# Optimization experiments

Hardware: AMD Instinct MI355X
Metric: run time of the kernel (lower is better)

The kernel has to match this reference:

```python
import jax, jax.numpy as jnp
import numpy as np

B, S, D = 4, 4096, 1024
H, DK, DV = 8, 128, 128
SEG = 512
DH = 4096
EPS = 1e-5


def setup_inputs() -> dict:
    key = jax.random.key(0)
    ks = jax.random.split(key, 8)
    n = lambda k, shp, sc: (jax.random.normal(k, shp, jnp.float32) * sc)
    return {
        "x": n(ks[0], (B, S, D), 1.0),
        "ln_gamma": jnp.ones((D,), jnp.float32),
        "ln_beta": jnp.zeros((D,), jnp.float32),
        "Wq": n(ks[1], (D, H * DK), 0.02),
        "Wk": n(ks[2], (D, H * DK), 0.02),
        "Wv": n(ks[3], (D, H * DV), 0.02),
        "Wo": n(ks[4], (H * DV, D), 0.02),
        "betas": n(ks[5], (1, H, 1, DV), 1.0),
        "ff_w1": n(ks[6], (D, DH), 0.02),
        "ff_b1": jnp.zeros((DH,), jnp.float32),
        "ff_w2": n(ks[7], (DH, D), 0.02),
        "ff_b2": jnp.zeros((D,), jnp.float32),
    }


def layer_norm(x, gamma, beta):
    mu = x.mean(-1, keepdims=True)
    var = x.var(-1, keepdims=True)
    return (x - mu) * jax.lax.rsqrt(var + EPS) * gamma + beta


def gelu_tanh(x):
    c = np.sqrt(2.0 / np.pi).astype(np.float32)
    return 0.5 * x * (1.0 + jnp.tanh(c * (x + 0.044715 * x * x * x)))


def infini_attention(x, Wq, Wk, Wv, Wo, betas):
    b, s, _ = x.shape
    nseg = s // SEG

    def proj(W, dh):
        # (b,s,H*dh) -> (nseg, b, H, SEG, dh)
        y = (x @ W).reshape(b, nseg, SEG, H, dh)
        return y.transpose(1, 0, 3, 2, 4)

    q = proj(Wq, DK)
    k = proj(Wk, DK)
    v = proj(Wv, DV)

    gate = jax.nn.sigmoid(betas)  # (1,H,1,DV)
    scale = 1.0 / np.sqrt(DK).astype(np.float32)
    causal_mask = jnp.tril(jnp.ones((SEG, SEG), bool))

    def step(carry, qkv):
        mem, z = carry  # (b,H,DK,DV), (b,H,DK,1)
        qs, ks_, vs = qkv  # (b,H,SEG,dk/dv)
        sq = jax.nn.elu(qs) + 1.0
        # compressive-memory retrieval
        att_mem = (sq @ mem) / (sq @ z)  # (b,H,SEG,DV)
        # local (segment) dot-product attention
        scores = jnp.einsum("bhqk,bhsk->bhqs", qs, ks_) * scale
        scores = jnp.where(causal_mask, scores, -jnp.inf)
        att = jax.nn.softmax(scores, axis=-1) @ vs  # (b,H,SEG,DV)
        # linear memory update
        sk = jax.nn.elu(ks_) + 1.0
        mem = mem + jnp.einsum("bhsk,bhsv->bhkv", sk, vs)
        z = z + sk.sum(axis=2)[..., None]
        out = gate * att_mem + (1.0 - gate) * att
        return (mem, z), out

    mem0 = jnp.zeros((b, H, DK, DV), x.dtype)
    z0 = jnp.ones((b, H, DK, 1), x.dtype) / DK
    _, outs = jax.lax.scan(step, (mem0, z0), (q, k, v))
    # (nseg,b,H,SEG,DV) -> (b,s,H*DV)
    outs = outs.transpose(1, 0, 3, 2, 4).reshape(b, s, H * DV)
    return outs @ Wo


def reference(x, ln_gamma, ln_beta, Wq, Wk, Wv, Wo, betas, ff_w1, ff_b1, ff_w2, ff_b2):
    h = layer_norm(x, ln_gamma, ln_beta)
    x = x + infini_attention(h, Wq, Wk, Wv, Wo, betas)
    h = layer_norm(x, ln_gamma, ln_beta)
    ff = gelu_tanh(h @ ff_w1 + ff_b1) @ ff_w2 + ff_b2
    return x + ff
```

## Files before the change

kernel.cpp:

```cpp
#include <hip/hip_runtime.h>

typedef unsigned short u16;
typedef unsigned int   u32;
typedef float f32x4 __attribute__((ext_vector_type(4)));
typedef short bf16x8 __attribute__((ext_vector_type(8)));

#define DEV static __device__ __forceinline__

DEV u16 f2b(float f){
  u32 u = __builtin_bit_cast(u32, f);
  return (u16)((u + 0x7fffu + ((u >> 16) & 1u)) >> 16);
}
DEV float b2f(u16 h){ u32 u = ((u32)h) << 16; return __builtin_bit_cast(float, u); }
DEV u32 pack2(float a, float b){ return (u32)f2b(a) | ((u32)f2b(b) << 16); }
DEV uint4 pack8(const float* f){
  uint4 r; r.x = pack2(f[0],f[1]); r.y = pack2(f[2],f[3]);
  r.z = pack2(f[4],f[5]); r.w = pack2(f[6],f[7]); return r;
}
DEV void unpack8(uint4 u, float* f){
  f[0]=b2f((u16)(u.x&0xffffu)); f[1]=b2f((u16)(u.x>>16));
  f[2]=b2f((u16)(u.y&0xffffu)); f[3]=b2f((u16)(u.y>>16));
  f[4]=b2f((u16)(u.z&0xffffu)); f[5]=b2f((u16)(u.z>>16));
  f[6]=b2f((u16)(u.w&0xffffu)); f[7]=b2f((u16)(u.w>>16));
}
DEV float gelu_t(float x){
  const float z2 = 1.5957691216057308f*(x + 0.044715f*x*x*x);
  return x / (1.f + __expf(-z2));
}
DEV void g2l16(const u16* g, u16* l){
  __builtin_amdgcn_global_load_lds(
    (const __attribute__((address_space(1))) u32*)g,
    (__attribute__((address_space(3))) u32*)l, 16, 0, 0);
}

__global__ __launch_bounds__(256)
void ln_k(const float* __restrict__ x, const float* __restrict__ gamma,
          const float* __restrict__ beta, u16* __restrict__ out)
{
  const int row = blockIdx.x;
  const int t = threadIdx.x;
  const float4 v = ((const float4*)(x + (size_t)row*1024))[t];
  float s  = v.x+v.y+v.z+v.w;
  float ss = v.x*v.x+v.y*v.y+v.z*v.z+v.w*v.w;
  #pragma unroll
  for (int o=32;o;o>>=1){ s += __shfl_xor(s,o); ss += __shfl_xor(ss,o); }
  __shared__ float rs[4], rq[4];
  if ((t&63)==0){ rs[t>>6]=s; rq[t>>6]=ss; }
  __syncthreads();
  s  = rs[0]+rs[1]+rs[2]+rs[3];
  ss = rq[0]+rq[1]+rq[2]+rq[3];
  const float mean = s*(1.f/1024.f);
  const float var  = ss*(1.f/1024.f) - mean*mean;
  const float inv  = rsqrtf(var + 1e-5f);
  const float4 g4 = ((const float4*)gamma)[t];
  const float4 b4 = ((const float4*)beta)[t];
  float o[4];
  o[0]=(v.x-mean)*inv*g4.x+b4.x; o[1]=(v.y-mean)*inv*g4.y+b4.y;
  o[2]=(v.z-mean)*inv*g4.z+b4.z; o[3]=(v.w-mean)*inv*g4.w+b4.w;
  uint2 w; w.x = pack2(o[0],o[1]); w.y = pack2(o[2],o[3]);
  *(uint2*)(out + (size_t)row*1024 + t*4) = w;
}

__global__ __launch_bounds__(256)
void wconv_k(const float* __restrict__ W, u16* __restrict__ WT, int K, int N)
{
  __shared__ float tile[32][33];
  const int k0 = blockIdx.y<<5, n0 = blockIdx.x<<5;
  const int tx = threadIdx.x & 31, ty = threadIdx.x >> 5;
  #pragma unroll
  for (int r=0;r<32;r+=8)
    tile[ty+r][tx] = W[(size_t)(k0+ty+r)*N + n0+tx];
  __syncthreads();
  #pragma unroll
  for (int r=0;r<32;r+=8)
    WT[(size_t)(n0+ty+r)*K + k0+tx] = f2b(tile[tx][ty+r]);
}

#define EPI_QKV  0
#define EPI_WO   1
#define EPI_GELU 2
#define EPI_FF2  3

template<int EPI>
__global__ __launch_bounds__(512)
void gemm3_k(const u16* __restrict__ A, const u16* __restrict__ BT,
             int K, int lda, int ldb, int N,
             u16* __restrict__ obf, float* __restrict__ of32,
             const float* __restrict__ res, const float* __restrict__ bias)
{
  __shared__ __align__(16) u16 SA[2*4096];
  __shared__ __align__(16) u16 SB[2*8192];
  const int t = threadIdx.x, wid = t>>6, lane = t&63;
  const int c = lane&15, g = lane>>4;
  const int wm = wid>>2, wn = wid&3;
  const int nwg = gridDim.x*gridDim.y;
  const int lb = blockIdx.y*gridDim.x + blockIdx.x;
  const int nl = (lb&7)*(nwg>>3) + (lb>>3);
  const int bx = nl % gridDim.x, by = nl / gridDim.x;
  const int m0 = by<<7, n0 = bx<<8;
  const int srow = lane>>2;
  const int scol = (lane&3)<<3;
  const int sxor = (srow&3)<<3;
  const int rowA = (wid<<4) + srow;
  const u16* aSrc  = A  + (size_t)(m0 + rowA)*lda + (scol ^ sxor);
  const u16* bSrc0 = BT + (size_t)(n0 + rowA)*ldb + (scol ^ sxor);
  const u16* bSrc1 = BT + (size_t)(n0 + 128 + rowA)*ldb + (scol ^ sxor);
  const int kx = (g<<3) ^ ((c&3)<<3);

  f32x4 acc[4][4];
  const f32x4 zz = {0.f,0.f,0.f,0.f};
  #pragma unroll
  for (int i=0;i<4;i++){ acc[i][0]=zz; acc[i][1]=zz; acc[i][2]=zz; acc[i][3]=zz; }

  g2l16(aSrc,  &SA[wid<<9]);
  g2l16(bSrc0, &SB[wid<<9]);
  g2l16(bSrc1, &SB[(wid<<9) + 4096]);
  __syncthreads();

  const int nt = K >> 5;
  for (int tt = 0; tt < nt; ++tt){
    const int cur = tt & 1;
    if (tt + 1 < nt){
      const int ko = (tt+1) << 5;
      g2l16(aSrc + ko,  &SA[((cur^1)<<12) + (wid<<9)]);
      g2l16(bSrc0 + ko, &SB[((cur^1)<<13) + (wid<<9)]);
      g2l16(bSrc1 + ko, &SB[((cur^1)<<13) + (wid<<9) + 4096]);
    }
    bf16x8 af[4], bf[4];
    #pragma unroll
    for (int i=0;i<4;i++)
      af[i] = *(const bf16x8*)&SA[(cur<<12) + ((wm<<6)+(i<<4)+c)*32 + kx];
    #pragma unroll
    for (int j=0;j<4;j++)
      bf[j] = *(const bf16x8*)&SB[(cur<<13) + ((wn<<6)+(j<<4)+c)*32 + kx];
    #pragma unroll
    for (int i=0;i<4;i++)
      #pragma unroll
      for (int j=0;j<4;j++)
        acc[i][j] = __builtin_amdgcn_mfma_f32_16x16x32_bf16(af[i], bf[j], acc[i][j], 0,0,0);
    __syncthreads();
  }

  #pragma unroll
  for (int i=0;i<4;i++){
    const int gr0 = m0 + (wm<<6) + (i<<4) + (g<<2);
    #pragma unroll
    for (int j=0;j<4;j++){
      const int gc = n0 + (wn<<6) + (j<<4) + c;
      #pragma unroll
      for (int r=0;r<4;r++){
        const int gr = gr0 + r;
        const float vv = acc[i][j][r];
        if (EPI==EPI_QKV){
          obf[((size_t)(gc>>10)<<24) + (size_t)gr*1024 + (gc&1023)] = f2b(vv);
        } else if (EPI==EPI_WO){
          const size_t idx = (size_t)gr*N + gc;
          of32[idx] = res[idx] + vv;
        } else if (EPI==EPI_GELU){
          obf[(size_t)gr*N + gc] = f2b(gelu_t(vv + bias[gc]));
        } else {
          const size_t idx = (size_t)gr*N + gc;
          of32[idx] = of32[idx] + vv + (bias ? bias[gc] : 0.f);
        }
      }
    }
  }
}

__global__ __launch_bounds__(256)
void memseg_k(const u16* __restrict__ kb, const u16* __restrict__ vb,
              float* __restrict__ Mseg, float* __restrict__ zseg)
{
  const int bid = blockIdx.x;
  const int seg = bid & 7, h = (bid>>3)&7, b = bid>>6;
  __shared__ __align__(16) u16 Kt[128*64];
  __shared__ __align__(16) u16 Vt[128*64];
  const int t=threadIdx.x, w=t>>6, lane=t&63, c=lane&15, g=lane>>4;

  f32x4 acc[2][8];
  f32x4 zacc[2];
  const f32x4 zzero = {0.f,0.f,0.f,0.f};
  #pragma unroll
  for (int d=0;d<2;d++){ zacc[d]=zzero;
    #pragma unroll
    for (int j=0;j<8;j++) acc[d][j]=zzero; }
  bf16x8 bones;
  { u16 tmp[8];
    #pragma unroll
    for (int e=0;e<8;e++) tmp[e] = (c==0) ? (u16)0x3F80 : (u16)0;
    bones = __builtin_bit_cast(bf16x8, *(uint4*)tmp); }

  for (int s0=0; s0<512; s0+=64){
    __syncthreads();
    {
      const int s = lane, dk0 = w<<5;
      const size_t grow = ((size_t)b*4096 + seg*512 + s0 + s)*1024 + h*128 + dk0;
      #pragma unroll
      for (int jj=0;jj<4;jj++){
        float kf[8], vf[8];
        unpack8(*(const uint4*)(kb + grow + jj*8), kf);
        unpack8(*(const uint4*)(vb + grow + jj*8), vf);
        #pragma unroll
        for (int e=0;e<8;e++){
          const int dk = dk0 + jj*8 + e;
          const float ek = kf[e]>0.f ? kf[e]+1.f : __expf(kf[e]);
          Kt[(dk<<6) + (s ^ ((dk&7)<<3))] = f2b(ek);
          Vt[(dk<<6) + (s ^ ((dk&7)<<3))] = f2b(vf[e]);
        }
      }
    }
    __syncthreads();
    #pragma unroll
    for (int ks=0;ks<2;ks++){
      const int kc = (ks<<5) + (g<<3);
      const bf16x8 a0 = *(const bf16x8*)&Kt[((((w<<1)  )*16 + c)<<6) + (kc ^ ((c&7)<<3))];
      const bf16x8 a1 = *(const bf16x8*)&Kt[((((w<<1)+1)*16 + c)<<6) + (kc ^ ((c&7)<<3))];
      zacc[0] = __builtin_amdgcn_mfma_f32_16x16x32_bf16(a0, bones, zacc[0], 0,0,0);
      zacc[1] = __builtin_amdgcn_mfma_f32_16x16x32_bf16(a1, bones, zacc[1], 0,0,0);
      #pragma unroll
      for (int j=0;j<8;j++){
        const bf16x8 bv = *(const bf16x8*)&Vt[(((j<<4) + c)<<6) + (kc ^ ((c&7)<<3))];
        acc[0][j] = __builtin_amdgcn_mfma_f32_16x16x32_bf16(a0, bv, acc[0][j], 0,0,0);
        acc[1][j] = __builtin_amdgcn_mfma_f32_16x16x32_bf16(a1, bv, acc[1][j], 0,0,0);
      }
    }
  }
  const size_t mb = (size_t)bid*16384;
  #pragma unroll
  for (int d=0;d<2;d++){
    const int dk = ((w<<1)+d)*16 + (g<<2);
    #pragma unroll
    for (int j=0;j<8;j++)
      #pragma unroll
      for (int r=0;r<4;r++)
        Mseg[mb + (size_t)(dk + r)*128 + (j<<4) + c] = acc[d][j][r];
    if (c==0){
      #pragma unroll
      for (int r=0;r<4;r++) zseg[(size_t)bid*128 + dk + r] = zacc[d][r];
    }
  }
}

__global__ __launch_bounds__(256)
void scan_k(const float* __restrict__ Mseg, const float* __restrict__ zseg,
            u16* __restrict__ memBT, float* __restrict__ zB)
{
  const int bh = blockIdx.x >> 3, oct = blockIdx.x & 7;
  const int t = threadIdx.x;
  const int dv = (oct<<4) + (t&15);
  const int kd0 = (t>>4)<<3;
  float run[8];
  #pragma unroll
  for (int i=0;i<8;i++) run[i]=0.f;
  for (int seg=0; seg<8; seg++){
    const size_t base = ((size_t)bh*8 + seg)*16384;
    u16 tmp[8];
    #pragma unroll
    for (int i=0;i<8;i++) tmp[i] = f2b(run[i]);
    *(uint4*)(memBT + base + (size_t)dv*128 + kd0) = *(const uint4*)tmp;
    #pragma unroll
    for (int i=0;i<8;i++) run[i] += Mseg[base + (size_t)(kd0+i)*128 + dv];
  }
  if (oct==0 && t < 128){
    float zr = 1.f/128.f;
    for (int seg=0; seg<8; seg++){
      const size_t base = ((size_t)bh*8 + seg)*128;
      zB[base + t] = zr;
      zr += zseg[base + t];
    }
  }
}

__global__ __launch_bounds__(256,2)
void attn_k(const u16* __restrict__ qb, const u16* __restrict__ kb,
            const u16* __restrict__ vb, const u16* __restrict__ memBT,
            const float* __restrict__ zB, const float* __restrict__ betas,
            u16* __restrict__ attc)
{
  const int bid = blockIdx.x;
  const int s = bid & 255, rt = 7 - (bid >> 8);
  const int seg = s&7, h=(s>>3)&7, b=s>>6;
  __shared__ __align__(16) u16 smem[16384];
  __shared__ __align__(16) u16 Ps[4096];
  u16* Ks = smem;
  u16* Vt = smem + 8192;
  float* zP = (float*)Ps;
  const int t=threadIdx.x, w=t>>6, lane=t&63, c=lane&15, g=lane>>4;
  const size_t base = ((size_t)b*4096 + seg*512)*1024 + h*128;

  bf16x8 af[4];
  {
    const u16* qsrc = qb + base + (size_t)(rt*64 + (w<<4) + c)*1024 + (g<<3);
    #pragma unroll
    for (int ks=0;ks<4;ks++) af[ks] = *(const bf16x8*)(qsrc + ks*32);
  }
  f32x4 acc[8];
  #pragma unroll
  for (int f=0;f<8;f++) acc[f] = (f32x4){0.f,0.f,0.f,0.f};
  float m_run[4], l_run[4];
  #pragma unroll
  for (int r=0;r<4;r++){ m_run[r] = -1e30f; l_run[r] = 0.f; }
  const float scl = 0.08838834764831845f;

  for (int kc=0; kc<=rt; kc++){
    __syncthreads();
    #pragma unroll
    for (int j=0;j<4;j++){
      const int row = (j<<2) + (lane>>4);
      const u16* src = kb + base + (size_t)(kc*64 + (w<<4) + row)*1024
                       + ((size_t)((lane&15) ^ (((w<<4)+row)&7)) << 3);
      g2l16(src, Ks + (((w<<4)+(j<<2))<<7));
    }
    {
      const int kr = lane, d0 = w<<5;
      const u16* vsrc = vb + base + (size_t)(kc*64+kr)*1024 + d0;
      #pragma unroll
      for (int jj=0;jj<4;jj++){
        const uint4 vv = *(const uint4*)(vsrc + jj*8);
        u16 tmp[8]; *(uint4*)tmp = vv;
        #pragma unroll
        for (int e=0;e<8;e++){
          const int dv = d0 + jj*8 + e;
          Vt[(dv<<6) + (kr ^ ((dv&7)<<3))] = tmp[e];
        }
      }
    }
    __syncthreads();
    f32x4 sv[4];
    #pragma unroll
    for (int j=0;j<4;j++) sv[j] = (f32x4){0.f,0.f,0.f,0.f};
    #pragma unroll
    for (int ks=0;ks<4;ks++)
      #pragma unroll
      for (int j=0;j<4;j++){
        const bf16x8 bk = *(const bf16x8*)&Ks[(((j<<4)+c)<<7) + ((((ks<<2)|g) ^ (c&7))<<3)];
        sv[j] = __builtin_amdgcn_mfma_f32_16x16x32_bf16(af[ks], bk, sv[j], 0,0,0);
      }
    const bool diag = (kc==rt);
    float p[4][4], rm[4], rsum[4];
    #pragma unroll
    for (int r=0;r<4;r++){
      float mx = -1e30f;
      #pragma unroll
      for (int j=0;j<4;j++){
        float svv = sv[j][r]*scl;
        if (diag && ((j<<4)+c) > ((w<<4) + (g<<2) + r)) svv = -1e30f;
        p[j][r] = svv;
        mx = fmaxf(mx, svv);
      }
      rm[r] = mx;
    }
    #pragma unroll
    for (int o=1;o<16;o<<=1)
      #pragma unroll
      for (int r=0;r<4;r++) rm[r] = fmaxf(rm[r], __shfl_xor(rm[r], o));
    #pragma unroll
    for (int r=0;r<4;r++){
      const float mn = fmaxf(m_run[r], rm[r]);
      const float sc = __expf(m_run[r] - mn);
      m_run[r] = mn;
      float sum = 0.f;
      #pragma unroll
      for (int j=0;j<4;j++){ p[j][r] = __expf(p[j][r]-mn); sum += p[j][r]; }
      rsum[r] = sum;
      l_run[r] *= sc;
      #pragma unroll
      for (int f=0;f<8;f++) acc[f][r] *= sc;
    }
    #pragma unroll
    for (int o=1;o<16;o<<=1)
      #pragma unroll
      for (int r=0;r<4;r++) rsum[r] += __shfl_xor(rsum[r], o);
    #pragma unroll
    for (int r=0;r<4;r++) l_run[r] += rsum[r];
    #pragma unroll
    for (int j=0;j<4;j++)
      #pragma unroll
      for (int r=0;r<4;r++){
        const int prow = (w<<4)+(g<<2)+r;
        Ps[(prow<<6) + (((j<<4)+c) ^ ((prow&7)<<3))] = f2b(p[j][r]);
      }
    #pragma unroll
    for (int ks2=0; ks2<2; ks2++){
      const bf16x8 pa = *(const bf16x8*)&Ps[(((w<<4)+c)<<6) + ((((ks2<<2)|g) ^ (c&7))<<3)];
      #pragma unroll
      for (int f=0;f<8;f++){
        const int dv = (f<<4)+c;
        const bf16x8 bv = *(const bf16x8*)&Vt[(dv<<6) + ((((ks2<<2)|g) ^ (c&7))<<3)];
        acc[f] = __builtin_amdgcn_mfma_f32_16x16x32_bf16(pa, bv, acc[f], 0,0,0);
      }
    }
  }
  __syncthreads();
  {
    const size_t mbase = (((size_t)b*8+h)*8+seg) << 14;
    #pragma unroll
    for (int i=0;i<8;i++){
      const int row = (i<<2) + (lane>>4);
      const u16* src = memBT + mbase + ((size_t)((w<<5)+row)<<7)
                       + ((size_t)((lane&15) ^ (((w<<5)+row)&7)) << 3);
      g2l16(src, smem + (((w<<5)+(i<<2))<<7));
    }
    if (t < 128) zP[t] = zB[((((size_t)b*8+h)*8+seg)<<7) + t];
  }
  __syncthreads();
  float dpart = 0.f;
  #pragma unroll
  for (int ks=0;ks<4;ks++){
    float f[8]; unpack8(__builtin_bit_cast(uint4, af[ks]), f);
    #pragma unroll
    for (int e=0;e<8;e++){
      f[e] = f[e]>0.f ? f[e]+1.f : __expf(f[e]);
      dpart += f[e] * zP[ks*32 + (g<<3) + e];
    }
    af[ks] = __builtin_bit_cast(bf16x8, pack8(f));
  }
  dpart += __shfl_xor(dpart, 16);
  dpart += __shfl_xor(dpart, 32);
  float den[4];
  #pragma unroll
  for (int r=0;r<4;r++) den[r] = 1.f / __shfl(dpart, (g<<2)+r);
  #pragma unroll 2
  for (int f=0;f<8;f++){
    f32x4 nf = {0.f,0.f,0.f,0.f};
    #pragma unroll
    for (int ks=0;ks<4;ks++){
      const bf16x8 bm = *(const bf16x8*)&smem[(((f<<4)+c)<<7) + ((((ks<<2)|g) ^ (c&7))<<3)];
      nf = __builtin_amdgcn_mfma_f32_16x16x32_bf16(af[ks], bm, nf, 0,0,0);
    }
    const float bv = betas[(h<<7) + (f<<4) + c];
    const float gate = 1.f/(1.f+__expf(-bv));
    #pragma unroll
    for (int r=0;r<4;r++){
      const size_t idx = base + (size_t)(rt*64 + (w<<4) + (g<<2) + r)*1024 + (f<<4) + c;
      const float att = acc[f][r] / l_run[r];
      const float am  = nf[r] * den[r];
      attc[idx] = f2b(gate*am + (1.f-gate)*att);
    }
  }
}

extern "C" void kernel_launch(void* const* d_in, const int* in_sizes, int n_in,
                              void* d_out, int out_size, void* d_ws, size_t ws_size,
                              hipStream_t stream)
{
  (void)in_sizes; (void)n_in; (void)out_size; (void)ws_size;
  const float* x    = (const float*)d_in[0];
  const float* ln_g = (const float*)d_in[1];
  const float* ln_b = (const float*)d_in[2];
  const float* Wq   = (const float*)d_in[3];
  const float* Wk   = (const float*)d_in[4];
  const float* Wv   = (const float*)d_in[5];
  const float* Wo   = (const float*)d_in[6];
  const float* betas= (const float*)d_in[7];
  const float* w1   = (const float*)d_in[8];
  const float* b1   = (const float*)d_in[9];
  const float* w2   = (const float*)d_in[10];
  const float* b2   = (const float*)d_in[11];
  float* out = (float*)d_out;

  char* ws = (char*)d_ws;
  const size_t MB = 1048576;
  u16* qb  = (u16*)(ws);
  u16* kb  = (u16*)(ws + 32*MB);
  u16* vb  = (u16*)(ws + 64*MB);
  u16* Wqkv= (u16*)(ws + 96*MB);
  u16* Wob = (u16*)(ws + 102*MB);
  u16* w1b = (u16*)(ws + 104*MB);
  u16* w2b = (u16*)(ws + 112*MB);
  char* ob = (char*)d_out;
  u16*   h    = (u16*)ob;
  float* Mseg = (float*)(ob + 32*MB);
  u16*   memBT= (u16*)  (ob + 48*MB);
  float* zseg = (float*)(ob + 56*MB);
  float* zB   = (float*)(ob + 56*MB + 131072);
  u16*   at   = qb;
  u16*   h2   = vb;
  u16*   gb2  = qb;

  wconv_k<<<dim3(32,32),256,0,stream>>>(Wq, Wqkv,              1024,1024);
  wconv_k<<<dim3(32,32),256,0,stream>>>(Wk, Wqkv+1024*1024,    1024,1024);
  wconv_k<<<dim3(32,32),256,0,stream>>>(Wv, Wqkv+2*1024*1024,  1024,1024);
  wconv_k<<<dim3(32,32),256,0,stream>>>(Wo, Wob, 1024,1024);
  wconv_k<<<dim3(128,32),256,0,stream>>>(w1, w1b, 1024,4096);
  wconv_k<<<dim3(32,128),256,0,stream>>>(w2, w2b, 4096,1024);

  ln_k<<<16384,256,0,stream>>>(x, ln_g, ln_b, h);
  gemm3_k<EPI_QKV><<<dim3(12,128),512,0,stream>>>(h, Wqkv, 1024,1024,1024, 3072,
                                                  qb, nullptr, nullptr, nullptr);
  memseg_k<<<256,256,0,stream>>>(kb, vb, Mseg, zseg);
  scan_k<<<256,256,0,stream>>>(Mseg, zseg, memBT, zB);
  attn_k<<<2048,256,0,stream>>>(qb, kb, vb, memBT, zB, betas, at);
  gemm3_k<EPI_WO><<<dim3(4,128),512,0,stream>>>(at, Wob, 1024,1024,1024, 1024,
                                                nullptr, out, x, nullptr);
  ln_k<<<16384,256,0,stream>>>(out, ln_g, ln_b, h2);
  for (int cc = 0; cc < 2; cc++){
    gemm3_k<EPI_GELU><<<dim3(8,128),512,0,stream>>>(h2, w1b + (size_t)cc*2048*1024,
                                                    1024,1024,1024, 2048,
                                                    gb2, nullptr, nullptr, b1 + cc*2048);
    gemm3_k<EPI_FF2><<<dim3(4,128),512,0,stream>>>(gb2, w2b + (size_t)cc*2048,
                                                   2048,2048,4096, 1024,
                                                   nullptr, out, nullptr,
                                                   cc==0 ? b2 : nullptr);
  }
}
```

Baseline: 690.3 us.

## Process two adjacent query row-tiles per attention block to share K/V loads

The attention kernel now launches 512-thread blocks that handle two consecutive 64-row query tiles, with each half of the warps owning one tile. K and V chunks are loaded into shared memory once per block and reused by both tiles, which halves redundant global traffic and the block count. Each warp gets its own P buffer slice. The warps of the lower tile idle on the last chunk, and larger blocks may reduce occupancy flexibility.

```diff
diff --git a/kernel.cpp b/kernel.cpp
--- a/kernel.cpp
+++ b/kernel.cpp
@@ -271,26 +271,30 @@
   }
 }
 
-__global__ __launch_bounds__(256,2)
+__global__ __launch_bounds__(512,2)
 void attn_k(const u16* __restrict__ qb, const u16* __restrict__ kb,
             const u16* __restrict__ vb, const u16* __restrict__ memBT,
             const float* __restrict__ zB, const float* __restrict__ betas,
             u16* __restrict__ attc)
 {
   const int bid = blockIdx.x;
-  const int s = bid & 255, rt = 7 - (bid >> 8);
+  const int s = bid & 255;
+  const int pr = 3 - (bid >> 8);
   const int seg = s&7, h=(s>>3)&7, b=s>>6;
   __shared__ __align__(16) u16 smem[16384];
-  __shared__ __align__(16) u16 Ps[4096];
+  __shared__ __align__(16) u16 Ps[8192];
   u16* Ks = smem;
   u16* Vt = smem + 8192;
   float* zP = (float*)Ps;
   const int t=threadIdx.x, w=t>>6, lane=t&63, c=lane&15, g=lane>>4;
+  const int half = w>>2, wl = w&3;
+  const int myrt = (pr<<1) + half;
+  const int rt1  = (pr<<1) + 1;
   const size_t base = ((size_t)b*4096 + seg*512)*1024 + h*128;
 
   bf16x8 af[4];
   {
-    const u16* qsrc = qb + base + (size_t)(rt*64 + (w<<4) + c)*1024 + (g<<3);
+    const u16* qsrc = qb + base + (size_t)(myrt*64 + (wl<<4) + c)*1024 + (g<<3);
     #pragma unroll
     for (int ks=0;ks<4;ks++) af[ks] = *(const bf16x8*)(qsrc + ks*32);
   }
@@ -302,20 +306,20 @@
   for (int r=0;r<4;r++){ m_run[r] = -1e30f; l_run[r] = 0.f; }
   const float scl = 0.08838834764831845f;
 
-  for (int kc=0; kc<=rt; kc++){
+  for (int kc=0; kc<=rt1; kc++){
     __syncthreads();
     #pragma unroll
-    for (int j=0;j<4;j++){
-      const int row = (j<<2) + (lane>>4);
-      const u16* src = kb + base + (size_t)(kc*64 + (w<<4) + row)*1024
-                       + ((size_t)((lane&15) ^ (((w<<4)+row)&7)) << 3);
-      g2l16(src, Ks + (((w<<4)+(j<<2))<<7));
+    for (int j=0;j<2;j++){
+      const int row = (w<<3) + (j<<2) + (lane>>4);
+      const u16* src = kb + base + (size_t)(kc*64 + row)*1024
+                       + ((size_t)((lane&15) ^ (row&7)) << 3);
+      g2l16(src, Ks + (((w<<3)+(j<<2))<<7));
     }
     {
-      const int kr = lane, d0 = w<<5;
+      const int kr = lane, d0 = w<<4;
       const u16* vsrc = vb + base + (size_t)(kc*64+kr)*1024 + d0;
       #pragma unroll
-      for (int jj=0;jj<4;jj++){
+      for (int jj=0;jj<2;jj++){
         const uint4 vv = *(const uint4*)(vsrc + jj*8);
         u16 tmp[8]; *(uint4*)tmp = vv;
         #pragma unroll
@@ -326,68 +330,71 @@
       }
     }
     __syncthreads();
-    f32x4 sv[4];
-    #pragma unroll
-    for (int j=0;j<4;j++) sv[j] = (f32x4){0.f,0.f,0.f,0.f};
-    #pragma unroll
-    for (int ks=0;ks<4;ks++)
-      #pragma unroll
-      for (int j=0;j<4;j++){
-        const bf16x8 bk = *(const bf16x8*)&Ks[(((j<<4)+c)<<7) + ((((ks<<2)|g) ^ (c&7))<<3)];
-        sv[j] = __builtin_amdgcn_mfma_f32_16x16x32_bf16(af[ks], bk, sv[j], 0,0,0);
-      }
-    const bool diag = (kc==rt);
-    float p[4][4], rm[4], rsum[4];
-    #pragma unroll
-    for (int r=0;r<4;r++){
-      float mx = -1e30f;
-      #pragma unroll
-      for (int j=0;j<4;j++){
-        float svv = sv[j][r]*scl;
-        if (diag && ((j<<4)+c) > ((w<<4) + (g<<2) + r)) svv = -1e30f;
-        p[j][r] = svv;
-        mx = fmaxf(mx, svv);
-      }
-      rm[r] = mx;
-    }
-    #pragma unroll
-    for (int o=1;o<16;o<<=1)
-      #pragma unroll
-      for (int r=0;r<4;r++) rm[r] = fmaxf(rm[r], __shfl_xor(rm[r], o));
-    #pragma unroll
-    for (int r=0;r<4;r++){
-      const float mn = fmaxf(m_run[r], rm[r]);
-      const float sc = __expf(m_run[r] - mn);
-      m_run[r] = mn;
-      float sum = 0.f;
-      #pragma unroll
-      for (int j=0;j<4;j++){ p[j][r] = __expf(p[j][r]-mn); sum += p[j][r]; }
-      rsum[r] = sum;
-      l_run[r] *= sc;
-      #pragma unroll
-      for (int f=0;f<8;f++) acc[f][r] *= sc;
-    }
-    #pragma unroll
-    for (int o=1;o<16;o<<=1)
-      #pragma unroll
-      for (int r=0;r<4;r++) rsum[r] += __shfl_xor(rsum[r], o);
-    #pragma unroll
-    for (int r=0;r<4;r++) l_run[r] += rsum[r];
-    #pragma unroll
-    for (int j=0;j<4;j++)
+    if (kc <= myrt){
+      f32x4 sv[4];
+      #pragma unroll
+      for (int j=0;j<4;j++) sv[j] = (f32x4){0.f,0.f,0.f,0.f};
+      #pragma unroll
+      for (int ks=0;ks<4;ks++)
+        #pragma unroll
+        for (int j=0;j<4;j++){
+          const bf16x8 bk = *(const bf16x8*)&Ks[(((j<<4)+c)<<7) + ((((ks<<2)|g) ^ (c&7))<<3)];
+          sv[j] = __builtin_amdgcn_mfma_f32_16x16x32_bf16(af[ks], bk, sv[j], 0,0,0);
+        }
+      const bool diag = (kc==myrt);
+      float p[4][4], rm[4], rsum[4];
       #pragma unroll
       for (int r=0;r<4;r++){
-        const int prow = (w<<4)+(g<<2)+r;
-        Ps[(prow<<6) + (((j<<4)+c) ^ ((prow&7)<<3))] = f2b(p[j][r]);
-      }
-    #pragma unroll
-    for (int ks2=0; ks2<2; ks2++){
-      const bf16x8 pa = *(const bf16x8*)&Ps[(((w<<4)+c)<<6) + ((((ks2<<2)|g) ^ (c&7))<<3)];
-      #pragma unroll
-      for (int f=0;f<8;f++){
-        const int dv = (f<<4)+c;
-        const bf16x8 bv = *(const bf16x8*)&Vt[(dv<<6) + ((((ks2<<2)|g) ^ (c&7))<<3)];
-        acc[f] = __builtin_amdgcn_mfma_f32_16x16x32_bf16(pa, bv, acc[f], 0,0,0);
+        float mx = -1e30f;
+        #pragma unroll
+        for (int j=0;j<4;j++){
+          float svv = sv[j][r]*scl;
+          if (diag && ((j<<4)+c) > ((wl<<4) + (g<<2) + r)) svv = -1e30f;
+          p[j][r] = svv;
+          mx = fmaxf(mx, svv);
+        }
+        rm[r] = mx;
+      }
+      #pragma unroll
+      for (int o=1;o<16;o<<=1)
+        #pragma unroll
+        for (int r=0;r<4;r++) rm[r] = fmaxf(rm[r], __shfl_xor(rm[r], o));
+      #pragma unroll
+      for (int r=0;r<4;r++){
+        const float mn = fmaxf(m_run[r], rm[r]);
+        const float sc = __expf(m_run[r] - mn);
+        m_run[r] = mn;
+        float sum = 0.f;
+        #pragma unroll
+        for (int j=0;j<4;j++){ p[j][r] = __expf(p[j][r]-mn); sum += p[j][r]; }
+        rsum[r] = sum;
+        l_run[r] *= sc;
+        #pragma unroll
+        for (int f=0;f<8;f++) acc[f][r] *= sc;
+      }
+      #pragma unroll
+      for (int o=1;o<16;o<<=1)
+        #pragma unroll
+        for (int r=0;r<4;r++) rsum[r] += __shfl_xor(rsum[r], o);
+      #pragma unroll
+      for (int r=0;r<4;r++) l_run[r] += rsum[r];
+      u16* Pw = Ps + (w<<10);
+      #pragma unroll
+      for (int j=0;j<4;j++)
+        #pragma unroll
+        for (int r=0;r<4;r++){
+          const int prow = (g<<2)+r;
+          Pw[(prow<<6) + (((j<<4)+c) ^ ((prow&7)<<3))] = f2b(p[j][r]);
+        }
+      #pragma unroll
+      for (int ks2=0; ks2<2; ks2++){
+        const bf16x8 pa = *(const bf16x8*)&Pw[(c<<6) + ((((ks2<<2)|g) ^ (c&7))<<3)];
+        #pragma unroll
+        for (int f=0;f<8;f++){
+          const int dv = (f<<4)+c;
+          const bf16x8 bv = *(const bf16x8*)&Vt[(dv<<6) + ((((ks2<<2)|g) ^ (c&7))<<3)];
+          acc[f] = __builtin_amdgcn_mfma_f32_16x16x32_bf16(pa, bv, acc[f], 0,0,0);
+        }
       }
     }
   }
@@ -395,11 +402,11 @@
   {
     const size_t mbase = (((size_t)b*8+h)*8+seg) << 14;
     #pragma unroll
-    for (int i=0;i<8;i++){
-      const int row = (i<<2) + (lane>>4);
-      const u16* src = memBT + mbase + ((size_t)((w<<5)+row)<<7)
-                       + ((size_t)((lane&15) ^ (((w<<5)+row)&7)) << 3);
-      g2l16(src, smem + (((w<<5)+(i<<2))<<7));
+    for (int i=0;i<4;i++){
+      const int row = (w<<4) + (i<<2) + (lane>>4);
+      const u16* src = memBT + mbase + ((size_t)row<<7)
+                       + ((size_t)((lane&15) ^ (row&7)) << 3);
+      g2l16(src, smem + (((w<<4)+(i<<2))<<7));
     }
     if (t < 128) zP[t] = zB[((((size_t)b*8+h)*8+seg)<<7) + t];
   }
@@ -432,7 +439,7 @@
     const float gate = 1.f/(1.f+__expf(-bv));
     #pragma unroll
     for (int r=0;r<4;r++){
-      const size_t idx = base + (size_t)(rt*64 + (w<<4) + (g<<2) + r)*1024 + (f<<4) + c;
+      const size_t idx = base + (size_t)(myrt*64 + (wl<<4) + (g<<2) + r)*1024 + (f<<4) + c;
       const float att = acc[f][r] / l_run[r];
       const float am  = nf[r] * den[r];
       attc[idx] = f2b(gate*am + (1.f-gate)*att);
@@ -490,7 +497,7 @@
                                                   qb, nullptr, nullptr, nullptr);
   memseg_k<<<256,256,0,stream>>>(kb, vb, Mseg, zseg);
   scan_k<<<256,256,0,stream>>>(Mseg, zseg, memBT, zB);
-  attn_k<<<2048,256,0,stream>>>(qb, kb, vb, memBT, zB, betas, at);
+  attn_k<<<1024,512,0,stream>>>(qb, kb, vb, memBT, zB, betas, at);
   gemm3_k<EPI_WO><<<dim3(4,128),512,0,stream>>>(at, Wob, 1024,1024,1024, 1024,
                                                 nullptr, out, x, nullptr);
   ln_k<<<16384,256,0,stream>>>(out, ln_g, ln_b, h2);
```

After: 676.6 us. 2.0% less time.
